# Kernel optimization log

Measured on AMD Instinct MI355X. Metric: run time of the kernel, lower is better.

## Reference

```python
import jax, jax.numpy as jnp
import numpy as np

D_MODEL, D_INNER, D_STATE, DT_RANK, D_CONV = 768, 1536, 16, 48, 4
B, L = 2, 2048


def setup_inputs() -> dict:
    key = jax.random.key(0)
    ks = jax.random.split(key, 8)
    s = 0.02
    return {
        "x": jax.random.normal(ks[0], (B, L, D_MODEL), jnp.float32),
        "norm_w": jnp.ones((D_MODEL,), jnp.float32),
        "in_proj_w": jax.random.normal(ks[1], (2 * D_INNER, D_MODEL), jnp.float32) * s,
        "conv_w": jax.random.normal(ks[2], (D_INNER, 1, D_CONV), jnp.float32) * s,
        "conv_b": jnp.zeros((D_INNER,), jnp.float32),
        "x_proj_w": jax.random.normal(ks[3], (DT_RANK + 2 * D_STATE, D_INNER), jnp.float32) * s,
        "dt_proj_w": jax.random.normal(ks[4], (D_INNER, DT_RANK), jnp.float32) * s,
        "dt_proj_b": jax.random.normal(ks[5], (D_INNER,), jnp.float32) * s,
        "A_log": jnp.broadcast_to(jnp.log(jnp.arange(1, D_STATE + 1, dtype=jnp.float32)), (D_INNER, D_STATE)).copy(),
        "D": jnp.ones((D_INNER,), jnp.float32),
        "out_proj_w": jax.random.normal(ks[6], (D_MODEL, D_INNER), jnp.float32) * s,
    }


def _mamba_block(x, norm_w, in_proj_w, conv_w, conv_b, x_proj_w,
                 dt_proj_w, dt_proj_b, A_log, D, out_proj_w):
    residual = x
    # RMSNorm
    h = x * jax.lax.rsqrt(jnp.mean(x * x, axis=-1, keepdims=True) + 1e-5) * norm_w
    # in_proj -> chunk into (hs, gate)
    xz = jnp.einsum('bld,ed->ble', h, in_proj_w)          # [B,L,2*Di]
    xh, z = jnp.split(xz, 2, axis=-1)                     # each [B,L,Di]
    # causal depthwise conv1d (kernel D_CONV) + SiLU
    xt = jnp.transpose(xh, (0, 2, 1))                     # [B,Di,L]
    xt = jnp.pad(xt, ((0, 0), (0, 0), (D_CONV - 1, 0)))
    xc = jax.lax.conv_general_dilated(xt, conv_w, (1,), 'VALID',
                                      feature_group_count=D_INNER)
    xc = jax.nn.silu(xc + conv_b[None, :, None])
    xc = jnp.transpose(xc, (0, 2, 1))                     # [B,L,Di]
    # x_proj -> (dt, B, C)
    proj = jnp.einsum('bld,ed->ble', xc, x_proj_w)        # [B,L,dt_rank+2N]
    dt, Bm, Cm = jnp.split(proj, [DT_RANK, DT_RANK + D_STATE], axis=-1)
    delta = jax.nn.softplus(jnp.einsum('blr,dr->bld', dt, dt_proj_w) + dt_proj_b)  # [B,L,Di]
    A = -jnp.exp(A_log)                                   # [Di,N]
    dA = jnp.exp(delta[..., None] * A)                    # [B,L,Di,N]
    dBx = delta[..., None] * Bm[:, :, None, :] * xc[..., None]  # [B,L,Di,N]
    # selective scan over the sequence axis
    def step(hst, inp):
        dA_t, dBx_t, C_t = inp                            # [B,Di,N],[B,Di,N],[B,N]
        hst = dA_t * hst + dBx_t
        y = jnp.einsum('bdn,bn->bd', hst, C_t)
        return hst, y
    h0 = jnp.zeros((x.shape[0], D_INNER, D_STATE), x.dtype)
    _, ys = jax.lax.scan(step, h0, (jnp.moveaxis(dA, 1, 0),
                                    jnp.moveaxis(dBx, 1, 0),
                                    jnp.moveaxis(Cm, 1, 0)))
    y = jnp.moveaxis(ys, 0, 1)                            # [B,L,Di]
    y = y + xc * D                                        # skip connection D
    y = y * jax.nn.silu(z)                                # gate
    out = jnp.einsum('bld,ed->ble', y, out_proj_w)        # [B,L,Dm]
    return residual + out, residual


def reference(x, norm_w, in_proj_w, conv_w, conv_b, x_proj_w,
              dt_proj_w, dt_proj_b, A_log, D, out_proj_w):
    return _mamba_block(x, norm_w, in_proj_w, conv_w, conv_b, x_proj_w,
                        dt_proj_w, dt_proj_b, A_log, D, out_proj_w)
```

## Files before the change

kernel.cpp:

```cpp
#include <hip/hip_runtime.h>
#include <cstdint>
#include <cstddef>

typedef __bf16 bf16_t;
typedef __bf16 bf16x8 __attribute__((ext_vector_type(8)));
typedef float  f32x4  __attribute__((ext_vector_type(4)));

#define D_MODEL 768
#define D_INNER 1536
#define D_STATE 16
#define DT_RANK 48
#define NB      2
#define SEQ     2048
#define NTOK    (NB*SEQ)
#define XPROJ_N (DT_RANK + 2*D_STATE)
#define LC      32
#define NCHUNK  (SEQ/LC)
#define XP_KS   4
#define XP_KC   (D_INNER/XP_KS)

#define N_INW (2*D_INNER*D_MODEL)
#define N_XPW (XPROJ_N*D_INNER)
#define N_DTW (D_INNER*DT_RANK)
#define N_OPW (D_MODEL*D_INNER)
#define N_CVT (N_INW+N_XPW+N_DTW+N_OPW)
#define CVT_BLOCKS (N_CVT/1024)

typedef __attribute__((address_space(1))) void gvoid_t;
typedef __attribute__((address_space(3))) void lvoid_t;
__device__ __forceinline__ void g2lds16(const bf16_t* g, bf16_t* l) {
    __builtin_amdgcn_global_load_lds((gvoid_t*)g, (lvoid_t*)l, 16, 0, 0);
}

__global__ __launch_bounds__(256)
void prep_kernel(const float* __restrict__ in_proj_w, bf16_t* __restrict__ w_in,
                 const float* __restrict__ x_proj_w,  bf16_t* __restrict__ w_xp,
                 const float* __restrict__ dt_proj_w, bf16_t* __restrict__ w_dt,
                 const float* __restrict__ out_proj_w,bf16_t* __restrict__ w_op,
                 const float* __restrict__ x, const float* __restrict__ norm_w,
                 bf16_t* __restrict__ h) {
    const int blk = blockIdx.x;
    const int tid = threadIdx.x;
    if (blk < CVT_BLOCKS) {
        int off = (blk * 256 + tid) * 4;
        const float* s; bf16_t* d;
        if (off < N_INW) { s = in_proj_w + off; d = w_in + off; }
        else if ((off -= N_INW) < N_XPW) { s = x_proj_w + off; d = w_xp + off; }
        else if ((off -= N_XPW) < N_DTW) { s = dt_proj_w + off; d = w_dt + off; }
        else { off -= N_DTW; s = out_proj_w + off; d = w_op + off; }
        float4 v = *(const float4*)s;
        d[0] = (bf16_t)v.x; d[1] = (bf16_t)v.y;
        d[2] = (bf16_t)v.z; d[3] = (bf16_t)v.w;
        return;
    }
    int t = blk - CVT_BLOCKS;
    const float* xr = x + (size_t)t * D_MODEL;
    float v[3];
    float ss = 0.f;
#pragma unroll
    for (int i = 0; i < 3; i++) { v[i] = xr[tid + 256*i]; ss += v[i]*v[i]; }
#pragma unroll
    for (int off = 32; off >= 1; off >>= 1) ss += __shfl_down(ss, off);
    __shared__ float red[4];
    int lane = tid & 63, wv = tid >> 6;
    if (lane == 0) red[wv] = ss;
    __syncthreads();
    float tot = red[0] + red[1] + red[2] + red[3];
    float r = rsqrtf(tot * (1.f/(float)D_MODEL) + 1e-5f);
#pragma unroll
    for (int i = 0; i < 3; i++)
        h[(size_t)t*D_MODEL + tid + 256*i] = (bf16_t)(v[i] * r * norm_w[tid + 256*i]);
}

__global__ __launch_bounds__(256)
void gemm_nt128(const bf16_t* __restrict__ A, int lda,
                const bf16_t* __restrict__ B, int ldb,
                bf16_t* __restrict__ C, int ldc, int K) {
    __shared__ __align__(16) bf16_t As[2][128*32];
    __shared__ __align__(16) bf16_t Bs[2][128*32];
    const int tid = threadIdx.x;
    const int wave = tid >> 6, lane = tid & 63;
    const int quad = lane >> 4, l16 = lane & 15;
    const int m0 = blockIdx.x * 128, n0 = blockIdx.y * 128;
    const int wr = (wave >> 1) * 64, wc = (wave & 1) * 64;

    const int s0 = tid, s1 = tid + 256;
    const int r0 = s0 >> 2, q0 = ((s0 & 3) ^ ((r0 >> 1) & 3)) << 3;
    const int r1 = s1 >> 2, q1 = ((s1 & 3) ^ ((r1 >> 1) & 3)) << 3;

    const bf16_t* Ar0 = A + (size_t)(m0 + r0)*lda + q0;
    const bf16_t* Ar1 = A + (size_t)(m0 + r1)*lda + q1;
    const bf16_t* Br0 = B + (size_t)(n0 + r0)*ldb + q0;
    const bf16_t* Br1 = B + (size_t)(n0 + r1)*ldb + q1;

    f32x4 acc[4][4] = {};
    const int nit = K >> 5;

    g2lds16(Ar0, &As[0][wave*512]);
    g2lds16(Ar1, &As[0][wave*512 + 2048]);
    g2lds16(Br0, &Bs[0][wave*512]);
    g2lds16(Br1, &Bs[0][wave*512 + 2048]);

    for (int it = 0; it < nit; it++) {
        __syncthreads();
        if (it + 1 < nit) {
            int k = (it + 1) << 5;
            int nb = (it + 1) & 1;
            g2lds16(Ar0 + k, &As[nb][wave*512]);
            g2lds16(Ar1 + k, &As[nb][wave*512 + 2048]);
            g2lds16(Br0 + k, &Bs[nb][wave*512]);
            g2lds16(Br1 + k, &Bs[nb][wave*512 + 2048]);
        }
        const int buf = it & 1;
        bf16x8 af[4], bfr[4];
#pragma unroll
        for (int i = 0; i < 4; i++) {
            int rr = wr + i*16 + l16;
            af[i] = *(const bf16x8*)&As[buf][rr*32 + ((quad ^ ((rr >> 1) & 3)) << 3)];
        }
#pragma unroll
        for (int j = 0; j < 4; j++) {
            int rr = wc + j*16 + l16;
            bfr[j] = *(const bf16x8*)&Bs[buf][rr*32 + ((quad ^ ((rr >> 1) & 3)) << 3)];
        }
#pragma unroll
        for (int i = 0; i < 4; i++)
#pragma unroll
            for (int j = 0; j < 4; j++)
                acc[i][j] = __builtin_amdgcn_mfma_f32_16x16x32_bf16(af[i], bfr[j], acc[i][j], 0, 0, 0);
    }

#pragma unroll
    for (int i = 0; i < 4; i++)
#pragma unroll
        for (int j = 0; j < 4; j++) {
            int n = n0 + wc + j*16 + l16;
#pragma unroll
            for (int rr = 0; rr < 4; rr++) {
                int m = m0 + wr + i*16 + quad*4 + rr;
                C[(size_t)m * ldc + n] = (bf16_t)acc[i][j][rr];
            }
        }
}

__global__ __launch_bounds__(256)
void gemm_op(const bf16_t* __restrict__ A, const bf16_t* __restrict__ B,
             float* __restrict__ C, const float* __restrict__ resid,
             float* __restrict__ resid_out) {
    __shared__ __align__(16) bf16_t As[2][128*32];
    __shared__ __align__(16) bf16_t Bs[2][64*32];
    const int tid = threadIdx.x;
    const int wave = tid >> 6, lane = tid & 63;
    const int quad = lane >> 4, l16 = lane & 15;
    const int m0 = blockIdx.x * 128, n0 = blockIdx.y * 64;
    const int wr = (wave >> 1) * 64, wc = (wave & 1) * 32;

    const int s0 = tid, s1 = tid + 256;
    const int r0 = s0 >> 2, q0 = ((s0 & 3) ^ ((r0 >> 1) & 3)) << 3;
    const int r1 = s1 >> 2, q1 = ((s1 & 3) ^ ((r1 >> 1) & 3)) << 3;
    const int rB = tid >> 2, qB = (((tid & 3) ^ ((rB >> 1) & 3)) << 3);

    const bf16_t* Ar0 = A + (size_t)(m0 + r0)*D_INNER + q0;
    const bf16_t* Ar1 = A + (size_t)(m0 + r1)*D_INNER + q1;
    const bf16_t* Brp = B + (size_t)(n0 + rB)*D_INNER + qB;

    f32x4 acc[4][2] = {};
    const int nit = D_INNER >> 5;

    g2lds16(Ar0, &As[0][wave*512]);
    g2lds16(Ar1, &As[0][wave*512 + 2048]);
    g2lds16(Brp, &Bs[0][wave*512]);

    for (int it = 0; it < nit; it++) {
        __syncthreads();
        if (it + 1 < nit) {
            int k = (it + 1) << 5;
            int nb = (it + 1) & 1;
            g2lds16(Ar0 + k, &As[nb][wave*512]);
            g2lds16(Ar1 + k, &As[nb][wave*512 + 2048]);
            g2lds16(Brp + k, &Bs[nb][wave*512]);
        }
        const int buf = it & 1;
        bf16x8 af[4], bfr[2];
#pragma unroll
        for (int i = 0; i < 4; i++) {
            int rr = wr + i*16 + l16;
            af[i] = *(const bf16x8*)&As[buf][rr*32 + ((quad ^ ((rr >> 1) & 3)) << 3)];
        }
#pragma unroll
        for (int j = 0; j < 2; j++) {
            int rr = wc + j*16 + l16;
            bfr[j] = *(const bf16x8*)&Bs[buf][rr*32 + ((quad ^ ((rr >> 1) & 3)) << 3)];
        }
#pragma unroll
        for (int i = 0; i < 4; i++)
#pragma unroll
            for (int j = 0; j < 2; j++)
                acc[i][j] = __builtin_amdgcn_mfma_f32_16x16x32_bf16(af[i], bfr[j], acc[i][j], 0, 0, 0);
    }

#pragma unroll
    for (int i = 0; i < 4; i++)
#pragma unroll
        for (int j = 0; j < 2; j++) {
            int n = n0 + wc + j*16 + l16;
#pragma unroll
            for (int rr = 0; rr < 4; rr++) {
                int m = m0 + wr + i*16 + quad*4 + rr;
                size_t idx = (size_t)m * D_MODEL + n;
                float rx = resid[idx];
                C[idx] = acc[i][j][rr] + rx;
                resid_out[idx] = rx;
            }
        }
}

__global__ __launch_bounds__(256)
void gemm_xp(const bf16_t* __restrict__ A, const bf16_t* __restrict__ B,
             float* __restrict__ pbuf) {
    __shared__ __align__(16) bf16_t As[64*32];
    __shared__ __align__(16) bf16_t Bs[64*32];
    const int tid = threadIdx.x;
    const int m0 = blockIdx.x * 64, n0 = blockIdx.y * 64, kbase = blockIdx.z * XP_KC;
    const int r  = tid >> 2, p8 = (tid & 3) << 3;
    const int q8 = (((tid & 3) ^ ((r >> 1) & 3)) << 3);
    const int wave = tid >> 6, lane = tid & 63;
    const int quad = lane >> 4, l16 = lane & 15;

    f32x4 acc[4] = {{0.f,0.f,0.f,0.f},{0.f,0.f,0.f,0.f},
                    {0.f,0.f,0.f,0.f},{0.f,0.f,0.f,0.f}};

    for (int k0 = 0; k0 < XP_KC; k0 += 32) {
        int gk = kbase + k0 + q8;
        uint4 va = *(const uint4*)(A + (size_t)(m0 + r) * D_INNER + gk);
        *(uint4*)&As[r*32 + p8] = va;
        uint4 vb = {0u,0u,0u,0u};
        int nr = n0 + r;
        if (nr < XPROJ_N)
            vb = *(const uint4*)(B + (size_t)nr * D_INNER + gk);
        *(uint4*)&Bs[r*32 + p8] = vb;

        __syncthreads();
        int ra = wave*16 + l16;
        bf16x8 af = *(const bf16x8*)&As[ra*32 + ((quad ^ ((ra >> 1) & 3)) << 3)];
#pragma unroll
        for (int nt = 0; nt < 4; nt++) {
            int rb = nt*16 + l16;
            bf16x8 bfg = *(const bf16x8*)&Bs[rb*32 + ((quad ^ ((rb >> 1) & 3)) << 3)];
            acc[nt] = __builtin_amdgcn_mfma_f32_16x16x32_bf16(af, bfg, acc[nt], 0, 0, 0);
        }
        __syncthreads();
    }

#pragma unroll
    for (int nt = 0; nt < 4; nt++) {
        int n = n0 + nt*16 + l16;
        if (n >= XPROJ_N) continue;
#pragma unroll
        for (int rr = 0; rr < 4; rr++) {
            int m = m0 + wave*16 + quad*4 + rr;
            pbuf[((size_t)blockIdx.z * NTOK + m) * XPROJ_N + n] = acc[nt][rr];
        }
    }
}

__global__ __launch_bounds__(256)
void xp_reduce_kernel(const float* __restrict__ pbuf, bf16_t* __restrict__ proj) {
    int i = blockIdx.x * 256 + threadIdx.x;
    if (i >= NTOK * XPROJ_N) return;
    float s = 0.f;
#pragma unroll
    for (int z = 0; z < XP_KS; z++)
        s += pbuf[(size_t)z * NTOK * XPROJ_N + i];
    proj[i] = (bf16_t)s;
}

__global__ __launch_bounds__(256)
void gemm_dt(const bf16_t* __restrict__ A, const bf16_t* __restrict__ B,
             bf16_t* __restrict__ C, const float* __restrict__ bias) {
    __shared__ __align__(16) bf16_t As[64*32];
    __shared__ __align__(16) bf16_t Bs[64*32];
    const int tid = threadIdx.x;
    const int m0 = blockIdx.x * 64, n0 = blockIdx.y * 64;
    const int r  = tid >> 2, p8 = (tid & 3) << 3;
    const int q8 = (((tid & 3) ^ ((r >> 1) & 3)) << 3);
    const int wave = tid >> 6, lane = tid & 63;
    const int quad = lane >> 4, l16 = lane & 15;

    f32x4 acc[4] = {{0.f,0.f,0.f,0.f},{0.f,0.f,0.f,0.f},
                    {0.f,0.f,0.f,0.f},{0.f,0.f,0.f,0.f}};

    for (int k0 = 0; k0 < DT_RANK; k0 += 32) {
        int gk = k0 + q8;
        uint4 va = {0u,0u,0u,0u};
        if (gk + 8 <= DT_RANK)
            va = *(const uint4*)(A + (size_t)(m0 + r) * XPROJ_N + gk);
        *(uint4*)&As[r*32 + p8] = va;
        uint4 vb = {0u,0u,0u,0u};
        if (gk + 8 <= DT_RANK)
            vb = *(const uint4*)(B + (size_t)(n0 + r) * DT_RANK + gk);
        *(uint4*)&Bs[r*32 + p8] = vb;

        __syncthreads();
        int ra = wave*16 + l16;
        bf16x8 af = *(const bf16x8*)&As[ra*32 + ((quad ^ ((ra >> 1) & 3)) << 3)];
#pragma unroll
        for (int nt = 0; nt < 4; nt++) {
            int rb = nt*16 + l16;
            bf16x8 bfg = *(const bf16x8*)&Bs[rb*32 + ((quad ^ ((rb >> 1) & 3)) << 3)];
            acc[nt] = __builtin_amdgcn_mfma_f32_16x16x32_bf16(af, bfg, acc[nt], 0, 0, 0);
        }
        __syncthreads();
    }

#pragma unroll
    for (int nt = 0; nt < 4; nt++) {
        int n = n0 + nt*16 + l16;
#pragma unroll
        for (int rr = 0; rr < 4; rr++) {
            int m = m0 + wave*16 + quad*4 + rr;
            float u = acc[nt][rr] + bias[n];
            float sp = (u > 20.f) ? u : log1pf(__expf(u));
            C[(size_t)m * D_INNER + n] = (bf16_t)sp;
        }
    }
}

__global__ __launch_bounds__(192)
void conv_silu_kernel(const bf16_t* __restrict__ xz,
                      const float* __restrict__ cw,
                      const float* __restrict__ cb,
                      bf16_t* __restrict__ xc) {
    const int t = blockIdx.x;
    const int l = t & (SEQ - 1);
    const int d = threadIdx.x * 8;

    float cwf[32];
#pragma unroll
    for (int q = 0; q < 8; q++)
        *(float4*)&cwf[q*4] = *(const float4*)&cw[d*4 + q*4];

    float acc[8];
    {
        float4 c0 = *(const float4*)&cb[d];
        float4 c1 = *(const float4*)&cb[d+4];
        acc[0]=c0.x; acc[1]=c0.y; acc[2]=c0.z; acc[3]=c0.w;
        acc[4]=c1.x; acc[5]=c1.y; acc[6]=c1.z; acc[7]=c1.w;
    }
#pragma unroll
    for (int k = 0; k < 4; k++) {
        if (l - 3 + k >= 0) {
            bf16x8 v = *(const bf16x8*)&xz[(size_t)(t - 3 + k) * (2*D_INNER) + d];
#pragma unroll
            for (int i = 0; i < 8; i++)
                acc[i] += (float)v[i] * cwf[i*4 + k];
        }
    }
    bf16x8 o;
#pragma unroll
    for (int i = 0; i < 8; i++) {
        float s = acc[i] / (1.f + __expf(-acc[i]));
        o[i] = (bf16_t)s;
    }
    *(bf16x8*)&xc[(size_t)t * D_INNER + d] = o;
}

__global__ __launch_bounds__(256)
void scan_part1(const bf16_t* __restrict__ delta,
                const bf16_t* __restrict__ xc,
                const bf16_t* __restrict__ proj,
                const float* __restrict__ A_log,
                float* __restrict__ chunk_h, float* __restrict__ chunk_P) {
    const int tid = threadIdx.x;
    const int d = blockIdx.x * 256 + tid;
    const int c = blockIdx.y;
    const int b = blockIdx.z;
    __shared__ float Bs[LC][D_STATE];
    for (int i = tid; i < LC*D_STATE; i += 256) {
        int l = i >> 4, n = i & 15;
        size_t t = (size_t)b*SEQ + (size_t)c*LC + l;
        Bs[l][n] = (float)proj[t*XPROJ_N + DT_RANK + n];
    }
    __syncthreads();
    float Av2[D_STATE];
#pragma unroll
    for (int n = 0; n < D_STATE; n++)
        Av2[n] = -__expf(A_log[d*D_STATE + n]) * 1.44269504f;
    float s[D_STATE];
#pragma unroll
    for (int n = 0; n < D_STATE; n++) s[n] = 0.f;
    float sdv = 0.f;
    const size_t tbase = (size_t)b*SEQ + (size_t)c*LC;
    for (int l = 0; l < LC; l++) {
        size_t t = tbase + l;
        float dv  = (float)delta[t*D_INNER + d];
        float xcv = (float)xc[t*D_INNER + d];
        float dx = dv * xcv;
        sdv += dv;
#pragma unroll
        for (int n = 0; n < D_STATE; n++) {
            float a = __builtin_amdgcn_exp2f(dv * Av2[n]);
            s[n] = a * s[n] + dx * Bs[l][n];
        }
    }
    size_t base = (((size_t)b*NCHUNK + c)*D_INNER + d)*D_STATE;
#pragma unroll
    for (int n = 0; n < D_STATE; n++) {
        chunk_h[base + n] = s[n];
        chunk_P[base + n] = __builtin_amdgcn_exp2f(Av2[n] * sdv);
    }
}

__global__ __launch_bounds__(256)
void scan_part2(float* __restrict__ chunk_h, const float* __restrict__ chunk_P) {
    int gid = blockIdx.x * 256 + threadIdx.x;
    int b  = gid / (D_INNER * D_STATE);
    int dn = gid - b * (D_INNER * D_STATE);
    float H = 0.f;
    for (int c = 0; c < NCHUNK; c++) {
        size_t idx = ((size_t)b*NCHUNK + c)*D_INNER*D_STATE + dn;
        float S = chunk_h[idx];
        float P = chunk_P[idx];
        chunk_h[idx] = H;
        H = P * H + S;
    }
}

__global__ __launch_bounds__(256)
void scan_part3(const bf16_t* __restrict__ delta,
                const bf16_t* __restrict__ xc,
                const bf16_t* __restrict__ proj,
                const bf16_t* __restrict__ xz,
                const float* __restrict__ A_log,
                const float* __restrict__ Dw,
                const float* __restrict__ chunk_h,
                bf16_t* __restrict__ y) {
    const int tid = threadIdx.x;
    const int d = blockIdx.x * 256 + tid;
    const int c = blockIdx.y;
    const int b = blockIdx.z;
    __shared__ float Bs[LC][D_STATE];
    __shared__ float Cs[LC][D_STATE];
    for (int i = tid; i < LC*D_STATE; i += 256) {
        int l = i >> 4, n = i & 15;
        size_t t = (size_t)b*SEQ + (size_t)c*LC + l;
        Bs[l][n] = (float)proj[t*XPROJ_N + DT_RANK + n];
        Cs[l][n] = (float)proj[t*XPROJ_N + DT_RANK + D_STATE + n];
    }
    __syncthreads();
    float Av2[D_STATE];
#pragma unroll
    for (int n = 0; n < D_STATE; n++)
        Av2[n] = -__expf(A_log[d*D_STATE + n]) * 1.44269504f;
    const float Dv = Dw[d];
    float s[D_STATE];
    size_t base = (((size_t)b*NCHUNK + c)*D_INNER + d)*D_STATE;
#pragma unroll
    for (int n = 0; n < D_STATE; n++) s[n] = chunk_h[base + n];
    const size_t tbase = (size_t)b*SEQ + (size_t)c*LC;
    for (int l = 0; l < LC; l++) {
        size_t t = tbase + l;
        float dv  = (float)delta[t*D_INNER + d];
        float xcv = (float)xc[t*D_INNER + d];
        float dx = dv * xcv;
        float acc = 0.f;
#pragma unroll
        for (int n = 0; n < D_STATE; n++) {
            float a = __builtin_amdgcn_exp2f(dv * Av2[n]);
            s[n] = a * s[n] + dx * Bs[l][n];
            acc += s[n] * Cs[l][n];
        }
        float zf = (float)xz[t*(2*D_INNER) + D_INNER + d];
        float g = zf / (1.f + __expf(-zf));
        y[t*D_INNER + d] = (bf16_t)((acc + xcv * Dv) * g);
    }
}

extern "C" void kernel_launch(void* const* d_in, const int* in_sizes, int n_in,
                              void* d_out, int out_size, void* d_ws, size_t ws_size,
                              hipStream_t stream) {
    const float* x          = (const float*)d_in[0];
    const float* norm_w     = (const float*)d_in[1];
    const float* in_proj_w  = (const float*)d_in[2];
    const float* conv_w     = (const float*)d_in[3];
    const float* conv_b     = (const float*)d_in[4];
    const float* x_proj_w   = (const float*)d_in[5];
    const float* dt_proj_w  = (const float*)d_in[6];
    const float* dt_proj_b  = (const float*)d_in[7];
    const float* A_log      = (const float*)d_in[8];
    const float* Dw         = (const float*)d_in[9];
    const float* out_proj_w = (const float*)d_in[10];

    float* out0 = (float*)d_out;
    float* out1 = out0 + (size_t)NTOK * D_MODEL;

    const size_t n_chunkst = (size_t)NB*NCHUNK*D_INNER*D_STATE;

    char* ws = (char*)d_ws;
    bf16_t* w_in  = (bf16_t*)ws;  ws += (size_t)N_INW * sizeof(bf16_t);
    bf16_t* w_xp  = (bf16_t*)ws;  ws += (size_t)N_XPW * sizeof(bf16_t);
    bf16_t* w_dt  = (bf16_t*)ws;  ws += (size_t)N_DTW * sizeof(bf16_t);
    bf16_t* w_op  = (bf16_t*)ws;  ws += (size_t)N_OPW * sizeof(bf16_t);
    bf16_t* h     = (bf16_t*)ws;  ws += (size_t)NTOK * D_MODEL   * sizeof(bf16_t);
    bf16_t* xz    = (bf16_t*)ws;  ws += (size_t)NTOK * 2*D_INNER * sizeof(bf16_t);
    bf16_t* xc    = (bf16_t*)ws;  ws += (size_t)NTOK * D_INNER   * sizeof(bf16_t);
    bf16_t* proj  = (bf16_t*)ws;  ws += (size_t)NTOK * XPROJ_N   * sizeof(bf16_t);
    bf16_t* delta = (bf16_t*)ws;  ws += (size_t)NTOK * D_INNER   * sizeof(bf16_t);
    bf16_t* y     = (bf16_t*)ws;  ws += (size_t)NTOK * D_INNER   * sizeof(bf16_t);
    float*  ch    = (float*)ws;   ws += n_chunkst * sizeof(float);
    float*  cP    = (float*)ws;   ws += n_chunkst * sizeof(float);
    float*  xppart= (float*)ws;   ws += (size_t)XP_KS * NTOK * XPROJ_N * sizeof(float);

    prep_kernel<<<CVT_BLOCKS + NTOK, 256, 0, stream>>>(
        in_proj_w, w_in, x_proj_w, w_xp, dt_proj_w, w_dt, out_proj_w, w_op,
        x, norm_w, h);
    gemm_nt128<<<dim3(NTOK/128, (2*D_INNER)/128), 256, 0, stream>>>(
        h, D_MODEL, w_in, D_MODEL, xz, 2*D_INNER, D_MODEL);
    conv_silu_kernel<<<NTOK, 192, 0, stream>>>(xz, conv_w, conv_b, xc);
    gemm_xp<<<dim3(NTOK/64, 2, XP_KS), 256, 0, stream>>>(xc, w_xp, xppart);
    xp_reduce_kernel<<<(NTOK*XPROJ_N + 255)/256, 256, 0, stream>>>(xppart, proj);
    gemm_dt<<<dim3(NTOK/64, D_INNER/64), 256, 0, stream>>>(proj, w_dt, delta, dt_proj_b);
    scan_part1<<<dim3(D_INNER/256, NCHUNK, NB), 256, 0, stream>>>(
        delta, xc, proj, A_log, ch, cP);
    scan_part2<<<(int)((size_t)NB*D_INNER*D_STATE/256), 256, 0, stream>>>(ch, cP);
    scan_part3<<<dim3(D_INNER/256, NCHUNK, NB), 256, 0, stream>>>(
        delta, xc, proj, xz, A_log, Dw, ch, y);
    gemm_op<<<dim3(NTOK/128, D_MODEL/64), 256, 0, stream>>>(
        y, w_op, out0, x, out1);
}
```

Measured before the change: 290.6 us.

## Split-K atomic out_proj, XCD block swizzle, batched conv rows, prefetched chunk scan

Several unrelated changes land together. The prep kernel now pre-writes the residual into both outputs. gemm_op becomes a 128x128 split-K (2-way) kernel that accumulates into out0 with float atomics. gemm_nt128 and gemm_op remap block IDs so that neighbouring tiles land on the same XCD for L2 reuse. The conv kernel handles 4 tokens per block and reuses the overlapping input rows. scan_part2 prefetches chunk states in groups of 8 to hide load latency. Atomic accumulation makes the output summation order nondeterministic and adds atomic traffic.

```diff
diff --git a/kernel.cpp b/kernel.cpp
--- a/kernel.cpp
+++ b/kernel.cpp
@@ -38,7 +38,8 @@
                  const float* __restrict__ dt_proj_w, bf16_t* __restrict__ w_dt,
                  const float* __restrict__ out_proj_w,bf16_t* __restrict__ w_op,
                  const float* __restrict__ x, const float* __restrict__ norm_w,
-                 bf16_t* __restrict__ h) {
+                 bf16_t* __restrict__ h,
+                 float* __restrict__ out0, float* __restrict__ out1) {
     const int blk = blockIdx.x;
     const int tid = threadIdx.x;
     if (blk < CVT_BLOCKS) {
@@ -68,8 +69,12 @@
     float tot = red[0] + red[1] + red[2] + red[3];
     float r = rsqrtf(tot * (1.f/(float)D_MODEL) + 1e-5f);
 #pragma unroll
-    for (int i = 0; i < 3; i++)
-        h[(size_t)t*D_MODEL + tid + 256*i] = (bf16_t)(v[i] * r * norm_w[tid + 256*i]);
+    for (int i = 0; i < 3; i++) {
+        size_t idx = (size_t)t*D_MODEL + tid + 256*i;
+        h[idx] = (bf16_t)(v[i] * r * norm_w[tid + 256*i]);
+        out0[idx] = v[i];
+        out1[idx] = v[i];
+    }
 }
 
 __global__ __launch_bounds__(256)
@@ -81,7 +86,11 @@
     const int tid = threadIdx.x;
     const int wave = tid >> 6, lane = tid & 63;
     const int quad = lane >> 4, l16 = lane & 15;
-    const int m0 = blockIdx.x * 128, n0 = blockIdx.y * 128;
+    const int nbx = gridDim.x, nby = gridDim.y;
+    int bid = blockIdx.y * nbx + blockIdx.x;
+    const int cpx = (nbx * nby) >> 3;
+    bid = (bid & 7) * cpx + (bid >> 3);
+    const int m0 = (bid / nby) * 128, n0 = (bid % nby) * 128;
     const int wr = (wave >> 1) * 64, wc = (wave & 1) * 64;
 
     const int s0 = tid, s1 = tid + 256;
@@ -145,31 +154,36 @@
 
 __global__ __launch_bounds__(256)
 void gemm_op(const bf16_t* __restrict__ A, const bf16_t* __restrict__ B,
-             float* __restrict__ C, const float* __restrict__ resid,
-             float* __restrict__ resid_out) {
+             float* __restrict__ C) {
     __shared__ __align__(16) bf16_t As[2][128*32];
-    __shared__ __align__(16) bf16_t Bs[2][64*32];
+    __shared__ __align__(16) bf16_t Bs[2][128*32];
     const int tid = threadIdx.x;
     const int wave = tid >> 6, lane = tid & 63;
     const int quad = lane >> 4, l16 = lane & 15;
-    const int m0 = blockIdx.x * 128, n0 = blockIdx.y * 64;
-    const int wr = (wave >> 1) * 64, wc = (wave & 1) * 32;
+    const int nbx = gridDim.x, nby = gridDim.y;
+    int bid = blockIdx.y * nbx + blockIdx.x;
+    const int cpx = (nbx * nby) >> 3;
+    bid = (bid & 7) * cpx + (bid >> 3);
+    const int m0 = (bid / nby) * 128, n0 = (bid % nby) * 128;
+    const int kbase = blockIdx.z * (D_INNER/2);
+    const int wr = (wave >> 1) * 64, wc = (wave & 1) * 64;
 
     const int s0 = tid, s1 = tid + 256;
     const int r0 = s0 >> 2, q0 = ((s0 & 3) ^ ((r0 >> 1) & 3)) << 3;
     const int r1 = s1 >> 2, q1 = ((s1 & 3) ^ ((r1 >> 1) & 3)) << 3;
-    const int rB = tid >> 2, qB = (((tid & 3) ^ ((rB >> 1) & 3)) << 3);
-
-    const bf16_t* Ar0 = A + (size_t)(m0 + r0)*D_INNER + q0;
-    const bf16_t* Ar1 = A + (size_t)(m0 + r1)*D_INNER + q1;
-    const bf16_t* Brp = B + (size_t)(n0 + rB)*D_INNER + qB;
-
-    f32x4 acc[4][2] = {};
-    const int nit = D_INNER >> 5;
+
+    const bf16_t* Ar0 = A + (size_t)(m0 + r0)*D_INNER + kbase + q0;
+    const bf16_t* Ar1 = A + (size_t)(m0 + r1)*D_INNER + kbase + q1;
+    const bf16_t* Br0 = B + (size_t)(n0 + r0)*D_INNER + kbase + q0;
+    const bf16_t* Br1 = B + (size_t)(n0 + r1)*D_INNER + kbase + q1;
+
+    f32x4 acc[4][4] = {};
+    const int nit = (D_INNER/2) >> 5;
 
     g2lds16(Ar0, &As[0][wave*512]);
     g2lds16(Ar1, &As[0][wave*512 + 2048]);
-    g2lds16(Brp, &Bs[0][wave*512]);
+    g2lds16(Br0, &Bs[0][wave*512]);
+    g2lds16(Br1, &Bs[0][wave*512 + 2048]);
 
     for (int it = 0; it < nit; it++) {
         __syncthreads();
@@ -178,39 +192,37 @@
             int nb = (it + 1) & 1;
             g2lds16(Ar0 + k, &As[nb][wave*512]);
             g2lds16(Ar1 + k, &As[nb][wave*512 + 2048]);
-            g2lds16(Brp + k, &Bs[nb][wave*512]);
+            g2lds16(Br0 + k, &Bs[nb][wave*512]);
+            g2lds16(Br1 + k, &Bs[nb][wave*512 + 2048]);
         }
         const int buf = it & 1;
-        bf16x8 af[4], bfr[2];
+        bf16x8 af[4], bfr[4];
 #pragma unroll
         for (int i = 0; i < 4; i++) {
             int rr = wr + i*16 + l16;
             af[i] = *(const bf16x8*)&As[buf][rr*32 + ((quad ^ ((rr >> 1) & 3)) << 3)];
         }
 #pragma unroll
-        for (int j = 0; j < 2; j++) {
+        for (int j = 0; j < 4; j++) {
             int rr = wc + j*16 + l16;
             bfr[j] = *(const bf16x8*)&Bs[buf][rr*32 + ((quad ^ ((rr >> 1) & 3)) << 3)];
         }
 #pragma unroll
         for (int i = 0; i < 4; i++)
 #pragma unroll
-            for (int j = 0; j < 2; j++)
+            for (int j = 0; j < 4; j++)
                 acc[i][j] = __builtin_amdgcn_mfma_f32_16x16x32_bf16(af[i], bfr[j], acc[i][j], 0, 0, 0);
     }
 
 #pragma unroll
     for (int i = 0; i < 4; i++)
 #pragma unroll
-        for (int j = 0; j < 2; j++) {
+        for (int j = 0; j < 4; j++) {
             int n = n0 + wc + j*16 + l16;
 #pragma unroll
             for (int rr = 0; rr < 4; rr++) {
                 int m = m0 + wr + i*16 + quad*4 + rr;
-                size_t idx = (size_t)m * D_MODEL + n;
-                float rx = resid[idx];
-                C[idx] = acc[i][j][rr] + rx;
-                resid_out[idx] = rx;
+                unsafeAtomicAdd(&C[(size_t)m * D_MODEL + n], acc[i][j][rr]);
             }
         }
 }
@@ -331,8 +343,8 @@
                       const float* __restrict__ cw,
                       const float* __restrict__ cb,
                       bf16_t* __restrict__ xc) {
-    const int t = blockIdx.x;
-    const int l = t & (SEQ - 1);
+    const int t0 = blockIdx.x * 4;
+    const int l0 = t0 & (SEQ - 1);
     const int d = threadIdx.x * 8;
 
     float cwf[32];
@@ -340,29 +352,39 @@
     for (int q = 0; q < 8; q++)
         *(float4*)&cwf[q*4] = *(const float4*)&cw[d*4 + q*4];
 
-    float acc[8];
-    {
-        float4 c0 = *(const float4*)&cb[d];
-        float4 c1 = *(const float4*)&cb[d+4];
-        acc[0]=c0.x; acc[1]=c0.y; acc[2]=c0.z; acc[3]=c0.w;
-        acc[4]=c1.x; acc[5]=c1.y; acc[6]=c1.z; acc[7]=c1.w;
-    }
-#pragma unroll
-    for (int k = 0; k < 4; k++) {
-        if (l - 3 + k >= 0) {
-            bf16x8 v = *(const bf16x8*)&xz[(size_t)(t - 3 + k) * (2*D_INNER) + d];
+    float cbv[8];
+    *(float4*)&cbv[0] = *(const float4*)&cb[d];
+    *(float4*)&cbv[4] = *(const float4*)&cb[d+4];
+
+    bf16x8 rows[7];
+#pragma unroll
+    for (int r = 0; r < 7; r++) {
+        if (l0 - 3 + r >= 0) {
+            rows[r] = *(const bf16x8*)&xz[(size_t)(t0 - 3 + r) * (2*D_INNER) + d];
+        } else {
+#pragma unroll
+            for (int i = 0; i < 8; i++) rows[r][i] = (bf16_t)0.f;
+        }
+    }
+
+#pragma unroll
+    for (int tt = 0; tt < 4; tt++) {
+        float acc[8];
+#pragma unroll
+        for (int i = 0; i < 8; i++) acc[i] = cbv[i];
+#pragma unroll
+        for (int k = 0; k < 4; k++)
 #pragma unroll
             for (int i = 0; i < 8; i++)
-                acc[i] += (float)v[i] * cwf[i*4 + k];
-        }
-    }
-    bf16x8 o;
-#pragma unroll
-    for (int i = 0; i < 8; i++) {
-        float s = acc[i] / (1.f + __expf(-acc[i]));
-        o[i] = (bf16_t)s;
-    }
-    *(bf16x8*)&xc[(size_t)t * D_INNER + d] = o;
+                acc[i] += (float)rows[tt + k][i] * cwf[i*4 + k];
+        bf16x8 o;
+#pragma unroll
+        for (int i = 0; i < 8; i++) {
+            float s = acc[i] / (1.f + __expf(-acc[i]));
+            o[i] = (bf16_t)s;
+        }
+        *(bf16x8*)&xc[(size_t)(t0 + tt) * D_INNER + d] = o;
+    }
 }
 
 __global__ __launch_bounds__(256)
@@ -416,13 +438,32 @@
     int gid = blockIdx.x * 256 + threadIdx.x;
     int b  = gid / (D_INNER * D_STATE);
     int dn = gid - b * (D_INNER * D_STATE);
+    const size_t cs = (size_t)D_INNER * D_STATE;
+    size_t base = (size_t)b * NCHUNK * cs + dn;
     float H = 0.f;
-    for (int c = 0; c < NCHUNK; c++) {
-        size_t idx = ((size_t)b*NCHUNK + c)*D_INNER*D_STATE + dn;
-        float S = chunk_h[idx];
-        float P = chunk_P[idx];
-        chunk_h[idx] = H;
-        H = P * H + S;
+    float S[8], P[8];
+#pragma unroll
+    for (int j = 0; j < 8; j++) {
+        S[j] = chunk_h[base + (size_t)j * cs];
+        P[j] = chunk_P[base + (size_t)j * cs];
+    }
+    for (int g = 0; g < 8; g++) {
+        float S2[8], P2[8];
+        if (g < 7) {
+#pragma unroll
+            for (int j = 0; j < 8; j++) {
+                S2[j] = chunk_h[base + (size_t)((g+1)*8 + j) * cs];
+                P2[j] = chunk_P[base + (size_t)((g+1)*8 + j) * cs];
+            }
+        }
+#pragma unroll
+        for (int j = 0; j < 8; j++) {
+            size_t idx = base + (size_t)(g*8 + j) * cs;
+            chunk_h[idx] = H;
+            H = fmaf(P[j], H, S[j]);
+        }
+#pragma unroll
+        for (int j = 0; j < 8; j++) { S[j] = S2[j]; P[j] = P2[j]; }
     }
 }
 
@@ -513,10 +554,10 @@
 
     prep_kernel<<<CVT_BLOCKS + NTOK, 256, 0, stream>>>(
         in_proj_w, w_in, x_proj_w, w_xp, dt_proj_w, w_dt, out_proj_w, w_op,
-        x, norm_w, h);
+        x, norm_w, h, out0, out1);
     gemm_nt128<<<dim3(NTOK/128, (2*D_INNER)/128), 256, 0, stream>>>(
         h, D_MODEL, w_in, D_MODEL, xz, 2*D_INNER, D_MODEL);
-    conv_silu_kernel<<<NTOK, 192, 0, stream>>>(xz, conv_w, conv_b, xc);
+    conv_silu_kernel<<<NTOK/4, 192, 0, stream>>>(xz, conv_w, conv_b, xc);
     gemm_xp<<<dim3(NTOK/64, 2, XP_KS), 256, 0, stream>>>(xc, w_xp, xppart);
     xp_reduce_kernel<<<(NTOK*XPROJ_N + 255)/256, 256, 0, stream>>>(xppart, proj);
     gemm_dt<<<dim3(NTOK/64, D_INNER/64), 256, 0, stream>>>(proj, w_dt, delta, dt_proj_b);
@@ -525,6 +566,5 @@
     scan_part2<<<(int)((size_t)NB*D_INNER*D_STATE/256), 256, 0, stream>>>(ch, cP);
     scan_part3<<<dim3(D_INNER/256, NCHUNK, NB), 256, 0, stream>>>(
         delta, xc, proj, xz, A_log, Dw, ch, y);
-    gemm_op<<<dim3(NTOK/128, D_MODEL/64), 256, 0, stream>>>(
-        y, w_op, out0, x, out1);
-}
+    gemm_op<<<dim3(NTOK/128, D_MODEL/128, 2), 256, 0, stream>>>(y, w_op, out0);
+}
```

Result: faster. 276.1 us (-5.0%).
